# Optimization experiments

Measured on AMD Instinct MI355X. Metric: run time of the kernel, lower is better.

## Reference

```python
import jax, jax.numpy as jnp
import numpy as np
import math

B, L = 2, 512
D_MODEL = 64
N_HEAD = 8
N_GLOBAL = 64
N_ITER = 2
DISTS = 4
K_RANK = 4
REG_H = 1.0
REG_Z = 1.0
NEG = -1e9


def setup_inputs() -> dict:
    key = jax.random.key(0)
    k1, k2, k3, k4 = jax.random.split(key, 4)
    x = jax.random.normal(k1, (B, L, D_MODEL), dtype=jnp.float32)
    mask = jnp.ones((B, L), dtype=jnp.int32)
    # nn.init.normal_ defaults (std=1)
    distribution_params = jax.random.normal(k2, (2 * DISTS, K_RANK), dtype=jnp.float32)
    ternary = jax.random.normal(k3, (K_RANK, D_MODEL, D_MODEL, N_HEAD), dtype=jnp.float32)
    # global_: std = 1/sqrt(d_model), single-channel -> heads dim = 1
    global_param = jax.random.normal(k4, (N_GLOBAL, D_MODEL, 1), dtype=jnp.float32) * (1.0 / math.sqrt(D_MODEL))
    return {"x": x, "mask": mask, "distribution_params": distribution_params,
            "ternary": ternary, "global_param": global_param}


def _softmax(s):
    return jax.nn.softmax(s, axis=-1)


def _distmask(distribution_params, n, dtype):
    # distance(i,j) = clip(i - j, -dists, dists); row 0 of params is zeros (distance 0)
    dist = jnp.arange(n)[:, None] - jnp.arange(n)[None, :]
    dist = jnp.clip(dist, -DISTS, DISTS)
    params = jnp.concatenate([jnp.zeros((1, K_RANK), dtype), distribution_params], axis=0)  # [2*dists+1, k]
    # torch negative indexing wraps; emulate explicitly
    idx = jnp.where(dist < 0, dist + 2 * DISTS + 1, dist)
    return params[idx].transpose(2, 0, 1)  # [k, n, n]


def reference(x, mask, distribution_params, ternary, global_param):
    bsz, n, d = x.shape
    mask1d = mask != 0                                   # [B, L]
    mask2d = mask1d[:, :, None] & mask1d[:, None, :]     # [B, L, L]
    inv2d = ~mask2d[:, None, :, :]                       # [B, 1, L, L] broadcast over heads
    inv1d = ~mask1d[:, None, :, None]                    # [B, 1, L, 1]

    distmask = _distmask(distribution_params, n, x.dtype)  # [k, L, L]

    unary = x
    q_z = unary
    for _ in range(N_ITER):
        # --- normalize Z beliefs (softmax over d_model states) ---
        Q_z = _softmax(q_z / REG_Z)                      # [B, L, d]
        # precompute decomposed tensor messages: M1[z,k,j,a,c] = sum_b Qz[z,j,b] T[k,a,b,c]
        M1 = jnp.einsum('zjb,kabc->zkjac', Q_z, ternary)  # [B, k, L, d, h]
        # --- H update (each head of token i picks a parent j) ---
        # s_h[z,c,i,j] = sum_{a,k} Qz[z,i,a] M1[z,k,j,a,c] distmask[k,i,j]
        s_h = jnp.einsum('zia,zkjac,kij->zcij', Q_z, M1, distmask)  # [B, h, L, L]
        s_h = jnp.where(inv2d, NEG, s_h)
        Q_h = _softmax(s_h / REG_H)                      # softmax over parents j
        # --- global H update (single channel): token i picks one of n_global global nodes ---
        s_g = jnp.einsum('zia,gac->zcig', Q_z, global_param)        # [B, 1, L, G]
        s_g = jnp.where(inv1d, NEG, s_g)
        Q_g = _softmax(s_g / REG_H)
        # --- Z update: messages from ternary factors in both roles + global factor ---
        g1 = jnp.einsum('zcij,zkjac,kij->zia', Q_h, M1, distmask)   # token as Z_i
        M2 = jnp.einsum('zjb,kbac->zkjac', Q_z, ternary)            # swapped roles
        g2 = jnp.einsum('zcji,zkjac,kji->zia', Q_h, M2, distmask)   # token as Z_j
        gg = jnp.einsum('zcig,gac->zia', Q_g, global_param)         # global message
        q_z = unary + g1 + g2 + gg
        # damping=0, stepsize=1 -> plain full update
    # output_prob=False -> unnormalized scores
    return q_z
```

## Files before the change

### kernel.cpp

```cpp
#include <hip/hip_runtime.h>

#define BB 2
#define LL 512
#define DD 64
#define HH 8
#define GG 64
#define KK 4
#define NEGV -1e9f
#define NSLOT 36

typedef unsigned short ushort_t;
typedef __attribute__((ext_vector_type(8))) short bf16x8;
typedef __attribute__((ext_vector_type(4))) float f32x4;
#define MFMA(a, b, c) __builtin_amdgcn_mfma_f32_16x16x32_bf16(a, b, c, 0, 0, 0)

typedef const __attribute__((address_space(1))) unsigned int* gptr_t;
typedef __attribute__((address_space(3))) unsigned int* lptr_t;

__device__ __forceinline__ ushort_t f2b(float f) {
    unsigned int u = __float_as_uint(f);
    return (ushort_t)((u + 0x7FFFu + ((u >> 16) & 1u)) >> 16);
}
__device__ __forceinline__ float b2f(ushort_t s) {
    return __uint_as_float(((unsigned int)s) << 16);
}

__device__ __forceinline__ void gll16(const ushort_t* g, const ushort_t* l) {
    __builtin_amdgcn_global_load_lds(
        (gptr_t)(unsigned long long)g,
        (lptr_t)(unsigned int)(unsigned long long)l,
        16, 0, 0);
}

__device__ __forceinline__ void stage64a(ushort_t* dst, const ushort_t* src,
                                         int rowstride, int tid) {
    int lane = tid & 63, w = tid >> 6;
#pragma unroll
    for (int h = 0; h < 2; ++h) {
        int g = h * 256 + w * 64 + lane;
        int row = g >> 3, colg = g & 7;
        gll16(src + (size_t)row * rowstride + ((colg ^ (row & 7)) << 3),
              dst + (size_t)(h * 256 + w * 64) * 8);
    }
}
__device__ __forceinline__ bf16x8 frag(const ushort_t* s, int row, int col) {
    return *reinterpret_cast<const bf16x8*>(&s[(row << 6) + ((((col >> 3) ^ (row & 7))) << 3)]);
}
__device__ __forceinline__ bf16x8 maskfrag(bf16x8 v, int cnt, bool keep_prefix) {
    bf16x8 r;
#pragma unroll
    for (int u = 0; u < 8; ++u) {
        bool keep = keep_prefix ? (u < cnt) : (u >= cnt);
        r[u] = keep ? v[u] : (short)0;
    }
    return r;
}
__device__ __forceinline__ int iclamp(int v, int lo, int hi) {
    return v < lo ? lo : (v > hi ? hi : v);
}

__global__ __launch_bounds__(256) void k_prepT(const float* __restrict__ T,
                                               ushort_t* __restrict__ TB1,
                                               ushort_t* __restrict__ TB2) {
    int k = blockIdx.x >> 3, c = blockIdx.x & 7;
    int tid = threadIdx.x;
    for (int g = tid; g < 512; g += 256) {
        int a = g >> 3, b0 = (g & 7) * 8;
        ushort_t o1[8], o2[8];
#pragma unroll
        for (int u = 0; u < 8; ++u) {
            o1[u] = f2b(T[(((k * 64 + a) * 64) + b0 + u) * 8 + c]);
            o2[u] = f2b(T[(((k * 64 + b0 + u) * 64) + a) * 8 + c]);
        }
        size_t base = ((size_t)(k * 8 + c) * 64 + a) * 64 + b0;
        *reinterpret_cast<uint4*>(&TB1[base]) = *reinterpret_cast<uint4*>(o1);
        *reinterpret_cast<uint4*>(&TB2[base]) = *reinterpret_cast<uint4*>(o2);
    }
}

__global__ __launch_bounds__(256) void k_softmax_qz(const float* __restrict__ src,
                                                    float* __restrict__ Qz,
                                                    ushort_t* __restrict__ QzB) {
    int row = blockIdx.x * 4 + (threadIdx.x >> 6);
    int lane = threadIdx.x & 63;
    float v = src[row * DD + lane];
    float m = v;
#pragma unroll
    for (int o = 32; o > 0; o >>= 1) m = fmaxf(m, __shfl_xor(m, o, 64));
    float e = __expf(v - m);
    float s = e;
#pragma unroll
    for (int o = 32; o > 0; o >>= 1) s += __shfl_xor(s, o, 64);
    float r = e / s;
    Qz[row * DD + lane] = r;
    QzB[row * DD + lane] = f2b(r);
}

__global__ __launch_bounds__(256) void k_compute_M(const ushort_t* __restrict__ QzB,
        const ushort_t* __restrict__ TB1, const ushort_t* __restrict__ TB2,
        ushort_t* __restrict__ M1Nb, ushort_t* __restrict__ M2Nb) {
    int jt = blockIdx.x, c = blockIdx.y;
    int z = blockIdx.z >> 2, k = blockIdx.z & 3;
    __shared__ __align__(16) ushort_t sQ[4096], sB1[4096], sB2[4096];
    int tid = threadIdx.x;
    stage64a(sQ, QzB + (size_t)(z * LL + jt * 64) * DD, DD, tid);
    size_t tb = (size_t)(k * 8 + c) * 4096;
    stage64a(sB1, TB1 + tb, 64, tid);
    stage64a(sB2, TB2 + tb, 64, tid);
    __syncthreads();
    int w = tid >> 6, lm = tid & 15, lg = (tid & 63) >> 4;
    f32x4 a1[4], a2[4];
#pragma unroll
    for (int nf = 0; nf < 4; ++nf) { a1[nf] = {0.f,0.f,0.f,0.f}; a2[nf] = {0.f,0.f,0.f,0.f}; }
#pragma unroll
    for (int ks = 0; ks < 2; ++ks) {
        int kc = ks * 32 + lg * 8;
        bf16x8 af = frag(sQ, w * 16 + lm, kc);
#pragma unroll
        for (int nf = 0; nf < 4; ++nf) {
            a1[nf] = MFMA(af, frag(sB1, nf * 16 + lm, kc), a1[nf]);
            a2[nf] = MFMA(af, frag(sB2, nf * 16 + lm, kc), a2[nf]);
        }
    }
    size_t base = (((size_t)z * KK + k) * HH + c) * LL;
#pragma unroll
    for (int nf = 0; nf < 4; ++nf)
#pragma unroll
        for (int r = 0; r < 4; ++r) {
            int j = jt * 64 + w * 16 + lg * 4 + r;
            int a = nf * 16 + lm;
            M1Nb[(base + j) * DD + a] = f2b(a1[nf][r]);
            M2Nb[(base + j) * DD + a] = f2b(a2[nf][r]);
        }
}

__global__ __launch_bounds__(256, 4) void k_collaux(const float* __restrict__ Qz,
        const ushort_t* __restrict__ M1Nb, const ushort_t* __restrict__ M2Nb,
        const float* __restrict__ dp, const float* __restrict__ gp, const int* __restrict__ mask,
        ushort_t* __restrict__ MPNb, ushort_t* __restrict__ MMNb,
        ushort_t* __restrict__ MP2Nb, ushort_t* __restrict__ MM2Nb,
        ushort_t* __restrict__ MPT, ushort_t* __restrict__ MMT,
        ushort_t* __restrict__ MP2T, ushort_t* __restrict__ MM2T,
        float* __restrict__ BAND, float* __restrict__ QG) {
    __shared__ __align__(16) ushort_t sT[4 * 64 * 65];
    int tid = threadIdx.x;
    int b = blockIdx.x;
    if (b < 128) {
        int jt = b & 7, zc = b >> 3;
        int z = zc >> 3, c = zc & 7;
        ushort_t* sP1 = sT;
        ushort_t* sM1 = sT + 64 * 65;
        ushort_t* sP2 = sT + 2 * 64 * 65;
        ushort_t* sM2 = sT + 3 * 64 * 65;
        float w4[4], w5[4];
#pragma unroll
        for (int k = 0; k < 4; ++k) { w4[k] = dp[12 + k]; w5[k] = dp[16 + k]; }
        size_t b0 = (((size_t)z * KK * HH + c) * LL + jt * 64) * DD;
        const size_t kstr = (size_t)HH * LL * DD;
        for (int g = tid; g < 512; g += 256) {
            int j = g >> 3, a0 = (g & 7) * 8;
            size_t o = b0 + (size_t)j * DD + a0;
            float p1[8] = {}, q1[8] = {}, p2[8] = {}, q2[8] = {};
#pragma unroll
            for (int k = 0; k < 4; ++k) {
                uint4 v1 = *reinterpret_cast<const uint4*>(&M1Nb[o + k * kstr]);
                uint4 v2 = *reinterpret_cast<const uint4*>(&M2Nb[o + k * kstr]);
                const ushort_t* s1 = reinterpret_cast<const ushort_t*>(&v1);
                const ushort_t* s2 = reinterpret_cast<const ushort_t*>(&v2);
#pragma unroll
                for (int u = 0; u < 8; ++u) {
                    float f1 = b2f(s1[u]), f2v = b2f(s2[u]);
                    p1[u] += w4[k] * f1; q1[u] += w5[k] * f1;
                    p2[u] += w4[k] * f2v; q2[u] += w5[k] * f2v;
                }
            }
            ushort_t t1[8], t2[8], t3[8], t4[8];
#pragma unroll
            for (int u = 0; u < 8; ++u) {
                t1[u] = f2b(p1[u]); t2[u] = f2b(q1[u]); t3[u] = f2b(p2[u]); t4[u] = f2b(q2[u]);
                sP1[(a0 + u) * 65 + j] = t1[u]; sM1[(a0 + u) * 65 + j] = t2[u];
                sP2[(a0 + u) * 65 + j] = t3[u]; sM2[(a0 + u) * 65 + j] = t4[u];
            }
            size_t on = ((size_t)zc * LL + jt * 64 + j) * DD + a0;
            *reinterpret_cast<uint4*>(&MPNb[on])  = *reinterpret_cast<uint4*>(t1);
            *reinterpret_cast<uint4*>(&MMNb[on])  = *reinterpret_cast<uint4*>(t2);
            *reinterpret_cast<uint4*>(&MP2Nb[on]) = *reinterpret_cast<uint4*>(t3);
            *reinterpret_cast<uint4*>(&MM2Nb[on]) = *reinterpret_cast<uint4*>(t4);
        }
        __syncthreads();
        for (int g = tid; g < 512; g += 256) {
            int a = g >> 3, j0 = (g & 7) * 8;
            ushort_t o1[8], o2[8], o3[8], o4[8];
#pragma unroll
            for (int u = 0; u < 8; ++u) {
                o1[u] = sP1[a * 65 + j0 + u]; o2[u] = sM1[a * 65 + j0 + u];
                o3[u] = sP2[a * 65 + j0 + u]; o4[u] = sM2[a * 65 + j0 + u];
            }
            size_t ot = ((size_t)zc * DD + a) * LL + jt * 64 + j0;
            *reinterpret_cast<uint4*>(&MPT[ot])  = *reinterpret_cast<uint4*>(o1);
            *reinterpret_cast<uint4*>(&MMT[ot])  = *reinterpret_cast<uint4*>(o2);
            *reinterpret_cast<uint4*>(&MP2T[ot]) = *reinterpret_cast<uint4*>(o3);
            *reinterpret_cast<uint4*>(&MM2T[ot]) = *reinterpret_cast<uint4*>(o4);
        }
    } else if (b < 2176) {
        int w = (b - 128) * 4 + (tid >> 6);
        int lane = tid & 63;
        int j = w & 511, c = (w >> 9) & 7, z = w >> 12;
        float m[4];
#pragma unroll
        for (int k = 0; k < 4; ++k)
            m[k] = b2f(M1Nb[((((size_t)z * KK + k) * HH + c) * LL + j) * DD + lane]);
        float out = 0.f;
#pragma unroll
        for (int d = -3; d <= 3; ++d) {
            int i = j + d;
            if (i < 0 || i >= LL) continue;
            int idx = d < 0 ? d + 9 : d;
            float t = 0.f;
            if (idx != 0) {
#pragma unroll
                for (int k = 0; k < 4; ++k) t += dp[(idx - 1) * 4 + k] * m[k];
            }
            float s = Qz[(z * LL + i) * DD + lane] * t;
#pragma unroll
            for (int o = 32; o > 0; o >>= 1) s += __shfl_xor(s, o, 64);
            if (lane == d + 3) out = s;
        }
        if (lane < 7) BAND[(size_t)w * 8 + lane] = out;
    } else {
        float* gpS = reinterpret_cast<float*>(sT);
#pragma unroll
        for (int idx = tid; idx < 4096; idx += 256) gpS[(idx >> 6) * 68 + (idx & 63)] = gp[idx];
        __syncthreads();
        int row = (b - 2176) * 4 + (tid >> 6);
        int g = tid & 63;
        float qv = Qz[row * DD + g];
        float s = 0.f;
#pragma unroll 8
        for (int a = 0; a < 64; ++a) s += __shfl(qv, a, 64) * gpS[g * 68 + a];
        if (mask[row] == 0) s = NEGV;
        float m = s;
#pragma unroll
        for (int o = 32; o > 0; o >>= 1) m = fmaxf(m, __shfl_xor(m, o, 64));
        float e = __expf(s - m);
        float sum = e;
#pragma unroll
        for (int o = 32; o > 0; o >>= 1) sum += __shfl_xor(sum, o, 64);
        QG[row * GG + g] = e / sum;
    }
}

__global__ __launch_bounds__(256, 2) void k_shsm32(const ushort_t* __restrict__ QzB,
        const ushort_t* __restrict__ MPNb, const ushort_t* __restrict__ MMNb,
        const float* __restrict__ BAND, const int* __restrict__ mask,
        ushort_t* __restrict__ SHB, ushort_t* __restrict__ SHBT) {
    int ih = blockIdx.x, zc = blockIdx.y;
    int it = ih >> 1, rh = ih & 1;
    int z = zc >> 3;
    int R0 = it * 64 + rh * 32;
    __shared__ __align__(16) ushort_t sA[2048];
    __shared__ __align__(16) ushort_t sB0[4096], sB1[4096], sBd[4096];
    __shared__ __align__(16) ushort_t tl[2][32 * 72];
    __shared__ float redA[2][32], redB[2][32];
    int tid = threadIdx.x;
    int w = tid >> 6, lm = tid & 15, lg = (tid & 63) >> 4;
    int rw = w & 1, cw = w >> 1;
    {
        int row = tid >> 3, colg = tid & 7;
        gll16(&QzB[(size_t)(z * LL + R0 + row) * DD + ((colg ^ (row & 7)) << 3)],
              sA + (size_t)(w * 64) * 8);
    }
    f32x4 acc[4][4];
#pragma unroll
    for (int jl = 0; jl < 4; ++jl)
#pragma unroll
        for (int nf = 0; nf < 4; ++nf) acc[jl][nf] = {0.f, 0.f, 0.f, 0.f};
    int dstep = it & 3;
#pragma unroll
    for (int s = 0; s < 4; ++s) {
        __syncthreads();
        int jt0 = s, jt1 = 4 + s;
        const ushort_t* src0 = (it >= jt0) ? MPNb : MMNb;
        const ushort_t* src1 = (it >= jt1) ? MPNb : MMNb;
        stage64a(sB0, src0 + ((size_t)zc * LL + jt0 * 64) * DD, DD, tid);
        stage64a(sB1, src1 + ((size_t)zc * LL + jt1 * 64) * DD, DD, tid);
        if (s == dstep)
            stage64a(sBd, MMNb + ((size_t)zc * LL + it * 64) * DD, DD, tid);
        __syncthreads();
        int jtg = cw ? jt1 : jt0;
        const ushort_t* sBx = cw ? sB1 : sB0;
#pragma unroll
        for (int ks = 0; ks < 2; ++ks) {
            int kc = ks * 32 + lg * 8;
            bf16x8 af = frag(sA, rw * 16 + lm, kc);
#pragma unroll
            for (int nf = 0; nf < 4; ++nf)
                acc[s][nf] = MFMA(af, frag(sBx, nf * 16 + lm, kc), acc[s][nf]);
        }
        if (jtg == it) {
            f32x4 accM[4];
#pragma unroll
            for (int nf = 0; nf < 4; ++nf) accM[nf] = {0.f, 0.f, 0.f, 0.f};
#pragma unroll
            for (int ks = 0; ks < 2; ++ks) {
                int kc = ks * 32 + lg * 8;
                bf16x8 af = frag(sA, rw * 16 + lm, kc);
#pragma unroll
                for (int nf = 0; nf < 4; ++nf)
                    accM[nf] = MFMA(af, frag(sBd, nf * 16 + lm, kc), accM[nf]);
            }
#pragma unroll
            for (int nf = 0; nf < 4; ++nf)
#pragma unroll
                for (int r = 0; r < 4; ++r) {
                    int i = R0 + rw * 16 + lg * 4 + r;
                    int j = it * 64 + nf * 16 + lm;
                    if (i <= j) acc[s][nf][r] = accM[nf][r];
                }
        }
    }
    int mi[4];
#pragma unroll
    for (int r = 0; r < 4; ++r) mi[r] = mask[z * LL + R0 + rw * 16 + lg * 4 + r];
#pragma unroll
    for (int jl = 0; jl < 4; ++jl) {
        int jtg = cw * 4 + jl;
#pragma unroll
        for (int nf = 0; nf < 4; ++nf) {
            int j = jtg * 64 + nf * 16 + lm;
            int mjv = mask[z * LL + j];
#pragma unroll
            for (int r = 0; r < 4; ++r) {
                int i = R0 + rw * 16 + lg * 4 + r;
                int d = i - j;
                float v = acc[jl][nf][r];
                if (d >= -3 && d <= 3) v = BAND[((size_t)zc * LL + j) * 8 + (d + 3)];
                if (!(mi[r] && mjv)) v = NEGV;
                acc[jl][nf][r] = v;
            }
        }
    }
    float gm[4], gs[4], inv[4];
#pragma unroll
    for (int r = 0; r < 4; ++r) {
        float m = -1e30f;
#pragma unroll
        for (int jl = 0; jl < 4; ++jl)
#pragma unroll
            for (int nf = 0; nf < 4; ++nf) m = fmaxf(m, acc[jl][nf][r]);
#pragma unroll
        for (int o = 1; o < 16; o <<= 1) m = fmaxf(m, __shfl_xor(m, o, 64));
        gm[r] = m;
    }
    if (lm == 0) {
#pragma unroll
        for (int r = 0; r < 4; ++r) redA[cw][rw * 16 + lg * 4 + r] = gm[r];
    }
    __syncthreads();
#pragma unroll
    for (int r = 0; r < 4; ++r)
        gm[r] = fmaxf(gm[r], redA[cw ^ 1][rw * 16 + lg * 4 + r]);
#pragma unroll
    for (int r = 0; r < 4; ++r) {
        float s = 0.f;
#pragma unroll
        for (int jl = 0; jl < 4; ++jl)
#pragma unroll
            for (int nf = 0; nf < 4; ++nf) {
                float e = __expf(acc[jl][nf][r] - gm[r]);
                acc[jl][nf][r] = e;
                s += e;
            }
#pragma unroll
        for (int o = 1; o < 16; o <<= 1) s += __shfl_xor(s, o, 64);
        gs[r] = s;
    }
    if (lm == 0) {
#pragma unroll
        for (int r = 0; r < 4; ++r) redB[cw][rw * 16 + lg * 4 + r] = gs[r];
    }
    __syncthreads();
#pragma unroll
    for (int r = 0; r < 4; ++r)
        inv[r] = 1.f / (gs[r] + redB[cw ^ 1][rw * 16 + lg * 4 + r]);
#pragma unroll
    for (int jl = 0; jl < 4; ++jl) {
        __syncthreads();
#pragma unroll
        for (int nf = 0; nf < 4; ++nf)
#pragma unroll
            for (int r = 0; r < 4; ++r)
                tl[cw][(rw * 16 + lg * 4 + r) * 72 + nf * 16 + lm] =
                    f2b(acc[jl][nf][r] * inv[r]);
        __syncthreads();
#pragma unroll
        for (int g = tid; g < 512; g += 256) {
            int cwg = g >> 8, rem = g & 255;
            int jtg = cwg * 4 + jl;
            int i_loc = rem >> 3, gj = rem & 7;
            ushort_t tmp[8];
#pragma unroll
            for (int u = 0; u < 8; ++u) tmp[u] = tl[cwg][i_loc * 72 + gj * 8 + u];
            *reinterpret_cast<uint4*>(
                &SHB[((size_t)zc * LL + R0 + i_loc) * LL + jtg * 64 + gj * 8]) =
                *reinterpret_cast<uint4*>(tmp);
        }
#pragma unroll
        for (int g = tid; g < 512; g += 256) {
            int cwg = g >> 8, rem = g & 255;
            int jtg = cwg * 4 + jl;
            int j_loc = rem >> 2, gi = rem & 3;
            ushort_t tmp2[8];
#pragma unroll
            for (int u = 0; u < 8; ++u) tmp2[u] = tl[cwg][(gi * 8 + u) * 72 + j_loc];
            *reinterpret_cast<uint4*>(
                &SHBT[((size_t)zc * LL + jtg * 64 + j_loc) * LL + R0 + gi * 8]) =
                *reinterpret_cast<uint4*>(tmp2);
        }
    }
}

__global__ __launch_bounds__(256, 4) void k_g12corr(const ushort_t* __restrict__ SHB,
        const ushort_t* __restrict__ SHBT,
        const ushort_t* __restrict__ MPT, const ushort_t* __restrict__ MMT,
        const ushort_t* __restrict__ MP2T, const ushort_t* __restrict__ MM2T,
        const ushort_t* __restrict__ M1Nb, const ushort_t* __restrict__ M2Nb,
        const ushort_t* __restrict__ MPNb, const ushort_t* __restrict__ MMNb,
        const ushort_t* __restrict__ MP2Nb, const ushort_t* __restrict__ MM2Nb,
        const float* __restrict__ dp, float* __restrict__ PG) {
    __shared__ __align__(16) ushort_t sSH[4096], sM[4096];
    int tid = threadIdx.x;
    int b = blockIdx.x;
    if (b < 512) {
        int it = b & 7, jc = (b >> 3) & 1, zcw = b >> 4;
        int which = zcw >> 4;
        int z = (zcw >> 3) & 1, c = zcw & 7;
        const ushort_t* Amat = which ? SHBT : SHB;
        const ushort_t* TP = which ? MP2T : MPT;
        const ushort_t* TM = which ? MM2T : MMT;
        int w = tid >> 6, lm = tid & 15, lg = (tid & 63) >> 4;
        f32x4 acc[4];
#pragma unroll
        for (int nf = 0; nf < 4; ++nf) acc[nf] = {0.f,0.f,0.f,0.f};
        size_t shbase = ((size_t)(z * HH + c) * LL + it * 64) * LL;
        size_t mbase  = ((size_t)(z * HH + c) * DD) * LL;
        for (int js = 0; js < 4; ++js) {
            int j0 = jc * 256 + js * 64;
            bool dg = (j0 == it * 64);
            bool useP = which == 0 ? (j0 < it * 64) : (j0 > it * 64);
            __syncthreads();
            stage64a(sSH, Amat + shbase + j0, LL, tid);
            stage64a(sM, (dg ? TP : (useP ? TP : TM)) + mbase + j0, LL, tid);
            __syncthreads();
            for (int pass = 0; pass < (dg ? 2 : 1); ++pass) {
                if (pass == 1) {
                    __syncthreads();
                    stage64a(sM, TM + mbase + j0, LL, tid);
                    __syncthreads();
                }
#pragma unroll
                for (int ks = 0; ks < 2; ++ks) {
                    int kc = ks * 32 + lg * 8;
                    int jb = j0 + kc;
                    bf16x8 af = frag(sSH, w * 16 + lm, kc);
                    if (dg) {
                        int i = it * 64 + w * 16 + lm;
                        int cnt = (which == 0) ? iclamp(i - jb, 0, 8) : iclamp(i + 1 - jb, 0, 8);
                        af = maskfrag(af, cnt, (pass == 0) == (which == 0));
                    }
#pragma unroll
                    for (int nf = 0; nf < 4; ++nf)
                        acc[nf] = MFMA(af, frag(sM, nf * 16 + lm, kc), acc[nf]);
                }
            }
        }
        int slot = which * 16 + c * 2 + jc;
#pragma unroll
        for (int nf = 0; nf < 4; ++nf)
#pragma unroll
            for (int r = 0; r < 4; ++r) {
                int i = it * 64 + w * 16 + lg * 4 + r;
                int a = nf * 16 + lm;
                PG[((size_t)(slot * BB + z) * LL + i) * DD + a] = acc[nf][r];
            }
    } else {
        int bid = b - 512;
        int which = bid >> 9; bid &= 511;
        int w = bid * 4 + (tid >> 6);
        int lane = tid & 63;
        int ch = w & 1, i = (w >> 1) & 511, z = w >> 10;
        const ushort_t* Mx = which ? M2Nb : M1Nb;
        const ushort_t* MPb = which ? MP2Nb : MPNb;
        const ushort_t* MMb = which ? MM2Nb : MMNb;
        float acc = 0.f;
        for (int cc = 0; cc < 4; ++cc) {
            int c = ch * 4 + cc;
#pragma unroll
            for (int d = -3; d <= 3; ++d) {
                int j = which ? i + d : i - d;
                if (j < 0 || j >= LL) continue;
                float qh = which ? b2f(SHB[(((size_t)z * HH + c) * LL + j) * LL + i])
                                 : b2f(SHB[(((size_t)z * HH + c) * LL + i) * LL + j]);
                int idx = d < 0 ? d + 9 : d;
                float e = 0.f;
                if (idx != 0) {
#pragma unroll
                    for (int k = 0; k < 4; ++k)
                        e += dp[(idx - 1) * 4 + k] *
                             b2f(Mx[((((size_t)z * KK + k) * HH + c) * LL + j) * DD + lane]);
                }
                const ushort_t* mb = (d > 0) ? MPb : MMb;
                float mn = b2f(mb[(((size_t)z * HH + c) * LL + j) * DD + lane]);
                acc += qh * (e - mn);
            }
        }
        int slot = 32 + which * 2 + ch;
        PG[(((size_t)slot * BB + z) * LL + i) * DD + lane] = acc;
    }
}

__global__ __launch_bounds__(256) void k_update_sm(const float* __restrict__ x,
                         const float* __restrict__ PG, const float* __restrict__ QG,
                         const float* __restrict__ gp,
                         float* __restrict__ Qz, ushort_t* __restrict__ QzB) {
    __shared__ __align__(16) float gpS[64][68];
    int tid = threadIdx.x;
#pragma unroll
    for (int idx = tid; idx < 4096; idx += 256) gpS[idx >> 6][idx & 63] = gp[idx];
    __syncthreads();
    int row = blockIdx.x * 4 + (tid >> 6);
    int a = tid & 63;
    float acc = x[row * DD + a];
    float qgv = QG[row * GG + a];
#pragma unroll 8
    for (int g = 0; g < 64; ++g) acc += __shfl(qgv, g, 64) * gpS[g][a];
#pragma unroll 6
    for (int s = 0; s < NSLOT; ++s) acc += PG[((size_t)s * BB * LL + row) * DD + a];
    float m = acc;
#pragma unroll
    for (int o = 32; o > 0; o >>= 1) m = fmaxf(m, __shfl_xor(m, o, 64));
    float e = __expf(acc - m);
    float s2 = e;
#pragma unroll
    for (int o = 32; o > 0; o >>= 1) s2 += __shfl_xor(s2, o, 64);
    float r = e / s2;
    Qz[row * DD + a] = r;
    QzB[row * DD + a] = f2b(r);
}

__global__ __launch_bounds__(256) void k_update_fin(const float* __restrict__ x,
                         const float* __restrict__ PG, const float* __restrict__ QG,
                         const float* __restrict__ gp, float* __restrict__ outq) {
    __shared__ __align__(16) float gpS[64][68];
    int tid = threadIdx.x;
#pragma unroll
    for (int idx = tid; idx < 4096; idx += 256) gpS[idx >> 6][idx & 63] = gp[idx];
    __syncthreads();
    int row = blockIdx.x * 4 + (tid >> 6);
    int a = tid & 63;
    float acc = x[row * DD + a];
    float qgv = QG[row * GG + a];
#pragma unroll 8
    for (int g = 0; g < 64; ++g) acc += __shfl(qgv, g, 64) * gpS[g][a];
#pragma unroll 6
    for (int s = 0; s < NSLOT; ++s) acc += PG[((size_t)s * BB * LL + row) * DD + a];
    outq[row * DD + a] = acc;
}

extern "C" void kernel_launch(void* const* d_in, const int* in_sizes, int n_in,
                              void* d_out, int out_size, void* d_ws, size_t ws_size,
                              hipStream_t stream) {
    const float* x    = (const float*)d_in[0];
    const int*   mask = (const int*)d_in[1];
    const float* dp   = (const float*)d_in[2];
    const float* T    = (const float*)d_in[3];
    const float* gp   = (const float*)d_in[4];
    float* out = (float*)d_out;

    float* p = (float*)d_ws;
    float* Qz = p;                        p += 65536;
    ushort_t* QzB = (ushort_t*)p;         p += 32768;
    ushort_t* TB1 = (ushort_t*)p;         p += 65536;
    ushort_t* TB2 = (ushort_t*)p;         p += 65536;
    ushort_t* M1Nb = (ushort_t*)p;        p += 1048576;
    ushort_t* M2Nb = (ushort_t*)p;        p += 1048576;
    ushort_t* MPNb  = (ushort_t*)p;       p += 262144;
    ushort_t* MMNb  = (ushort_t*)p;       p += 262144;
    ushort_t* MP2Nb = (ushort_t*)p;       p += 262144;
    ushort_t* MM2Nb = (ushort_t*)p;       p += 262144;
    ushort_t* MPT   = (ushort_t*)p;       p += 262144;
    ushort_t* MMT   = (ushort_t*)p;       p += 262144;
    ushort_t* MP2T  = (ushort_t*)p;       p += 262144;
    ushort_t* MM2T  = (ushort_t*)p;       p += 262144;
    float* BAND = p;                      p += 65536;
    ushort_t* SHB  = (ushort_t*)p;        p += 2097152;
    ushort_t* SHBT = (ushort_t*)p;        p += 2097152;
    float* QG   = p;                      p += 65536;
    float* PG   = p;                      p += (size_t)NSLOT * 65536;

    hipLaunchKernelGGL(k_prepT, dim3(32), dim3(256), 0, stream, T, TB1, TB2);
    hipLaunchKernelGGL(k_softmax_qz, dim3(256), dim3(256), 0, stream, x, Qz, QzB);

    for (int iter = 0; iter < 2; ++iter) {
        hipLaunchKernelGGL(k_compute_M, dim3(8, 8, 8), dim3(256), 0, stream, QzB, TB1, TB2, M1Nb, M2Nb);
        hipLaunchKernelGGL(k_collaux, dim3(2432), dim3(256), 0, stream, Qz, M1Nb, M2Nb, dp, gp, mask,
                           MPNb, MMNb, MP2Nb, MM2Nb, MPT, MMT, MP2T, MM2T, BAND, QG);
        hipLaunchKernelGGL(k_shsm32, dim3(16, 16), dim3(256), 0, stream, QzB, MPNb, MMNb, BAND, mask,
                           SHB, SHBT);
        hipLaunchKernelGGL(k_g12corr, dim3(1536), dim3(256), 0, stream, SHB, SHBT,
                           MPT, MMT, MP2T, MM2T, M1Nb, M2Nb,
                           MPNb, MMNb, MP2Nb, MM2Nb, dp, PG);
        if (iter == 0)
            hipLaunchKernelGGL(k_update_sm, dim3(256), dim3(256), 0, stream, x, PG, QG, gp, Qz, QzB);
        else
            hipLaunchKernelGGL(k_update_fin, dim3(256), dim3(256), 0, stream, x, PG, QG, gp, out);
    }
}
```

Measured before the change: 134.4 us.

## Fuse M computation with k-collapse and double-buffer LDS staging in downstream kernels

Merges the M1/M2 MFMA kernel with the k-weighted collapse into one kernel. Each block loops over the four ranks, accumulates the distance-weighted sums in registers, and writes both the normal and transposed collapsed tensors, so M1/M2 no longer have to be reread from global memory. The band/global-score work moves into a separate smaller kernel. It also adds double-buffered LDS prefetching in k_shsm32 and k_g12corr, which drops one barrier per step, and flattens the diagonal two-pass case into a linear subtile schedule. The cost is fewer blocks in the fused kernel (128) and more LDS per block.

```diff
diff --git a/kernel.cpp b/kernel.cpp
--- a/kernel.cpp
+++ b/kernel.cpp
@@ -96,114 +96,120 @@
     QzB[row * DD + lane] = f2b(r);
 }
 
-__global__ __launch_bounds__(256) void k_compute_M(const ushort_t* __restrict__ QzB,
+__global__ __launch_bounds__(256, 2) void k_Mcoll(const ushort_t* __restrict__ QzB,
         const ushort_t* __restrict__ TB1, const ushort_t* __restrict__ TB2,
-        ushort_t* __restrict__ M1Nb, ushort_t* __restrict__ M2Nb) {
-    int jt = blockIdx.x, c = blockIdx.y;
-    int z = blockIdx.z >> 2, k = blockIdx.z & 3;
-    __shared__ __align__(16) ushort_t sQ[4096], sB1[4096], sB2[4096];
-    int tid = threadIdx.x;
-    stage64a(sQ, QzB + (size_t)(z * LL + jt * 64) * DD, DD, tid);
-    size_t tb = (size_t)(k * 8 + c) * 4096;
-    stage64a(sB1, TB1 + tb, 64, tid);
-    stage64a(sB2, TB2 + tb, 64, tid);
-    __syncthreads();
-    int w = tid >> 6, lm = tid & 15, lg = (tid & 63) >> 4;
-    f32x4 a1[4], a2[4];
-#pragma unroll
-    for (int nf = 0; nf < 4; ++nf) { a1[nf] = {0.f,0.f,0.f,0.f}; a2[nf] = {0.f,0.f,0.f,0.f}; }
-#pragma unroll
-    for (int ks = 0; ks < 2; ++ks) {
-        int kc = ks * 32 + lg * 8;
-        bf16x8 af = frag(sQ, w * 16 + lm, kc);
-#pragma unroll
-        for (int nf = 0; nf < 4; ++nf) {
-            a1[nf] = MFMA(af, frag(sB1, nf * 16 + lm, kc), a1[nf]);
-            a2[nf] = MFMA(af, frag(sB2, nf * 16 + lm, kc), a2[nf]);
-        }
-    }
-    size_t base = (((size_t)z * KK + k) * HH + c) * LL;
-#pragma unroll
-    for (int nf = 0; nf < 4; ++nf)
-#pragma unroll
-        for (int r = 0; r < 4; ++r) {
-            int j = jt * 64 + w * 16 + lg * 4 + r;
-            int a = nf * 16 + lm;
-            M1Nb[(base + j) * DD + a] = f2b(a1[nf][r]);
-            M2Nb[(base + j) * DD + a] = f2b(a2[nf][r]);
-        }
-}
-
-__global__ __launch_bounds__(256, 4) void k_collaux(const float* __restrict__ Qz,
-        const ushort_t* __restrict__ M1Nb, const ushort_t* __restrict__ M2Nb,
-        const float* __restrict__ dp, const float* __restrict__ gp, const int* __restrict__ mask,
+        const float* __restrict__ dp,
+        ushort_t* __restrict__ M1Nb, ushort_t* __restrict__ M2Nb,
         ushort_t* __restrict__ MPNb, ushort_t* __restrict__ MMNb,
         ushort_t* __restrict__ MP2Nb, ushort_t* __restrict__ MM2Nb,
         ushort_t* __restrict__ MPT, ushort_t* __restrict__ MMT,
-        ushort_t* __restrict__ MP2T, ushort_t* __restrict__ MM2T,
+        ushort_t* __restrict__ MP2T, ushort_t* __restrict__ MM2T) {
+    int jt = blockIdx.x, zc = blockIdx.y;
+    int z = zc >> 3, c = zc & 7;
+    __shared__ __align__(16) ushort_t smem[20480];
+    ushort_t* sQ = smem;
+    int tid = threadIdx.x;
+    stage64a(sQ, QzB + (size_t)(z * LL + jt * 64) * DD, DD, tid);
+    stage64a(smem + 4096,  TB1 + (size_t)(0 * 8 + c) * 4096, 64, tid);
+    stage64a(smem + 12288, TB2 + (size_t)(0 * 8 + c) * 4096, 64, tid);
+    int w = tid >> 6, lm = tid & 15, lg = (tid & 63) >> 4;
+    float w4[4], w5[4];
+#pragma unroll
+    for (int k = 0; k < 4; ++k) { w4[k] = dp[12 + k]; w5[k] = dp[16 + k]; }
+    f32x4 cp1[4], cm1[4], cp2[4], cm2[4];
+#pragma unroll
+    for (int nf = 0; nf < 4; ++nf) {
+        cp1[nf] = {0.f,0.f,0.f,0.f}; cm1[nf] = {0.f,0.f,0.f,0.f};
+        cp2[nf] = {0.f,0.f,0.f,0.f}; cm2[nf] = {0.f,0.f,0.f,0.f};
+    }
+#pragma unroll
+    for (int k = 0; k < 4; ++k) {
+        __syncthreads();
+        if (k < 3) {
+            ushort_t* nb1 = smem + (((k + 1) & 1) ? 8192 : 4096);
+            ushort_t* nb2 = smem + (((k + 1) & 1) ? 16384 : 12288);
+            stage64a(nb1, TB1 + (size_t)((k + 1) * 8 + c) * 4096, 64, tid);
+            stage64a(nb2, TB2 + (size_t)((k + 1) * 8 + c) * 4096, 64, tid);
+        }
+        const ushort_t* b1 = smem + ((k & 1) ? 8192 : 4096);
+        const ushort_t* b2 = smem + ((k & 1) ? 16384 : 12288);
+        f32x4 a1[4], a2[4];
+#pragma unroll
+        for (int nf = 0; nf < 4; ++nf) { a1[nf] = {0.f,0.f,0.f,0.f}; a2[nf] = {0.f,0.f,0.f,0.f}; }
+#pragma unroll
+        for (int ks = 0; ks < 2; ++ks) {
+            int kc = ks * 32 + lg * 8;
+            bf16x8 af = frag(sQ, w * 16 + lm, kc);
+#pragma unroll
+            for (int nf = 0; nf < 4; ++nf) {
+                a1[nf] = MFMA(af, frag(b1, nf * 16 + lm, kc), a1[nf]);
+                a2[nf] = MFMA(af, frag(b2, nf * 16 + lm, kc), a2[nf]);
+            }
+        }
+        size_t base = (((size_t)z * KK + k) * HH + c) * LL;
+#pragma unroll
+        for (int nf = 0; nf < 4; ++nf)
+#pragma unroll
+            for (int r = 0; r < 4; ++r) {
+                int j = jt * 64 + w * 16 + lg * 4 + r;
+                int a = nf * 16 + lm;
+                float v1 = a1[nf][r], v2 = a2[nf][r];
+                M1Nb[(base + j) * DD + a] = f2b(v1);
+                M2Nb[(base + j) * DD + a] = f2b(v2);
+                cp1[nf][r] += w4[k] * v1; cm1[nf][r] += w5[k] * v1;
+                cp2[nf][r] += w4[k] * v2; cm2[nf][r] += w5[k] * v2;
+            }
+    }
+#pragma unroll
+    for (int nf = 0; nf < 4; ++nf)
+#pragma unroll
+        for (int r = 0; r < 4; ++r) {
+            int jl = w * 16 + lg * 4 + r;
+            int a = nf * 16 + lm;
+            size_t on = ((size_t)zc * LL + jt * 64 + jl) * DD + a;
+            MPNb[on]  = f2b(cp1[nf][r]); MMNb[on]  = f2b(cm1[nf][r]);
+            MP2Nb[on] = f2b(cp2[nf][r]); MM2Nb[on] = f2b(cm2[nf][r]);
+        }
+    __syncthreads();
+    ushort_t* tr0 = smem;
+    ushort_t* tr1 = smem + 4224;
+    ushort_t* tr2 = smem + 8448;
+    ushort_t* tr3 = smem + 12672;
+#pragma unroll
+    for (int nf = 0; nf < 4; ++nf)
+#pragma unroll
+        for (int r = 0; r < 4; ++r) {
+            int jl = w * 16 + lg * 4 + r;
+            int a = nf * 16 + lm;
+            tr0[a * 66 + jl] = f2b(cp1[nf][r]); tr1[a * 66 + jl] = f2b(cm1[nf][r]);
+            tr2[a * 66 + jl] = f2b(cp2[nf][r]); tr3[a * 66 + jl] = f2b(cm2[nf][r]);
+        }
+    __syncthreads();
+    for (int g = tid; g < 512; g += 256) {
+        int a = g >> 3, j0 = (g & 7) * 8;
+        ushort_t o1[8], o2[8], o3[8], o4[8];
+#pragma unroll
+        for (int u = 0; u < 8; ++u) {
+            o1[u] = tr0[a * 66 + j0 + u]; o2[u] = tr1[a * 66 + j0 + u];
+            o3[u] = tr2[a * 66 + j0 + u]; o4[u] = tr3[a * 66 + j0 + u];
+        }
+        size_t ot = ((size_t)zc * DD + a) * LL + jt * 64 + j0;
+        *reinterpret_cast<uint4*>(&MPT[ot])  = *reinterpret_cast<uint4*>(o1);
+        *reinterpret_cast<uint4*>(&MMT[ot])  = *reinterpret_cast<uint4*>(o2);
+        *reinterpret_cast<uint4*>(&MP2T[ot]) = *reinterpret_cast<uint4*>(o3);
+        *reinterpret_cast<uint4*>(&MM2T[ot]) = *reinterpret_cast<uint4*>(o4);
+    }
+}
+
+__global__ __launch_bounds__(256, 4) void k_bandqg(const float* __restrict__ Qz,
+        const ushort_t* __restrict__ M1Nb,
+        const float* __restrict__ dp, const float* __restrict__ gp, const int* __restrict__ mask,
         float* __restrict__ BAND, float* __restrict__ QG) {
-    __shared__ __align__(16) ushort_t sT[4 * 64 * 65];
+    __shared__ __align__(16) float gpS[64 * 68];
     int tid = threadIdx.x;
     int b = blockIdx.x;
-    if (b < 128) {
-        int jt = b & 7, zc = b >> 3;
-        int z = zc >> 3, c = zc & 7;
-        ushort_t* sP1 = sT;
-        ushort_t* sM1 = sT + 64 * 65;
-        ushort_t* sP2 = sT + 2 * 64 * 65;
-        ushort_t* sM2 = sT + 3 * 64 * 65;
-        float w4[4], w5[4];
-#pragma unroll
-        for (int k = 0; k < 4; ++k) { w4[k] = dp[12 + k]; w5[k] = dp[16 + k]; }
-        size_t b0 = (((size_t)z * KK * HH + c) * LL + jt * 64) * DD;
-        const size_t kstr = (size_t)HH * LL * DD;
-        for (int g = tid; g < 512; g += 256) {
-            int j = g >> 3, a0 = (g & 7) * 8;
-            size_t o = b0 + (size_t)j * DD + a0;
-            float p1[8] = {}, q1[8] = {}, p2[8] = {}, q2[8] = {};
-#pragma unroll
-            for (int k = 0; k < 4; ++k) {
-                uint4 v1 = *reinterpret_cast<const uint4*>(&M1Nb[o + k * kstr]);
-                uint4 v2 = *reinterpret_cast<const uint4*>(&M2Nb[o + k * kstr]);
-                const ushort_t* s1 = reinterpret_cast<const ushort_t*>(&v1);
-                const ushort_t* s2 = reinterpret_cast<const ushort_t*>(&v2);
-#pragma unroll
-                for (int u = 0; u < 8; ++u) {
-                    float f1 = b2f(s1[u]), f2v = b2f(s2[u]);
-                    p1[u] += w4[k] * f1; q1[u] += w5[k] * f1;
-                    p2[u] += w4[k] * f2v; q2[u] += w5[k] * f2v;
-                }
-            }
-            ushort_t t1[8], t2[8], t3[8], t4[8];
-#pragma unroll
-            for (int u = 0; u < 8; ++u) {
-                t1[u] = f2b(p1[u]); t2[u] = f2b(q1[u]); t3[u] = f2b(p2[u]); t4[u] = f2b(q2[u]);
-                sP1[(a0 + u) * 65 + j] = t1[u]; sM1[(a0 + u) * 65 + j] = t2[u];
-                sP2[(a0 + u) * 65 + j] = t3[u]; sM2[(a0 + u) * 65 + j] = t4[u];
-            }
-            size_t on = ((size_t)zc * LL + jt * 64 + j) * DD + a0;
-            *reinterpret_cast<uint4*>(&MPNb[on])  = *reinterpret_cast<uint4*>(t1);
-            *reinterpret_cast<uint4*>(&MMNb[on])  = *reinterpret_cast<uint4*>(t2);
-            *reinterpret_cast<uint4*>(&MP2Nb[on]) = *reinterpret_cast<uint4*>(t3);
-            *reinterpret_cast<uint4*>(&MM2Nb[on]) = *reinterpret_cast<uint4*>(t4);
-        }
-        __syncthreads();
-        for (int g = tid; g < 512; g += 256) {
-            int a = g >> 3, j0 = (g & 7) * 8;
-            ushort_t o1[8], o2[8], o3[8], o4[8];
-#pragma unroll
-            for (int u = 0; u < 8; ++u) {
-                o1[u] = sP1[a * 65 + j0 + u]; o2[u] = sM1[a * 65 + j0 + u];
-                o3[u] = sP2[a * 65 + j0 + u]; o4[u] = sM2[a * 65 + j0 + u];
-            }
-            size_t ot = ((size_t)zc * DD + a) * LL + jt * 64 + j0;
-            *reinterpret_cast<uint4*>(&MPT[ot])  = *reinterpret_cast<uint4*>(o1);
-            *reinterpret_cast<uint4*>(&MMT[ot])  = *reinterpret_cast<uint4*>(o2);
-            *reinterpret_cast<uint4*>(&MP2T[ot]) = *reinterpret_cast<uint4*>(o3);
-            *reinterpret_cast<uint4*>(&MM2T[ot]) = *reinterpret_cast<uint4*>(o4);
-        }
-    } else if (b < 2176) {
-        int w = (b - 128) * 4 + (tid >> 6);
+    if (b < 2048) {
+        int w = b * 4 + (tid >> 6);
         int lane = tid & 63;
         int j = w & 511, c = (w >> 9) & 7, z = w >> 12;
         float m[4];
@@ -228,11 +234,10 @@
         }
         if (lane < 7) BAND[(size_t)w * 8 + lane] = out;
     } else {
-        float* gpS = reinterpret_cast<float*>(sT);
 #pragma unroll
         for (int idx = tid; idx < 4096; idx += 256) gpS[(idx >> 6) * 68 + (idx & 63)] = gp[idx];
         __syncthreads();
-        int row = (b - 2176) * 4 + (tid >> 6);
+        int row = (b - 2048) * 4 + (tid >> 6);
         int g = tid & 63;
         float qv = Qz[row * DD + g];
         float s = 0.f;
@@ -259,7 +264,8 @@
     int z = zc >> 3;
     int R0 = it * 64 + rh * 32;
     __shared__ __align__(16) ushort_t sA[2048];
-    __shared__ __align__(16) ushort_t sB0[4096], sB1[4096], sBd[4096];
+    __shared__ __align__(16) ushort_t sBd[4096];
+    __shared__ __align__(16) ushort_t sB[2][8192];
     __shared__ __align__(16) ushort_t tl[2][32 * 72];
     __shared__ float redA[2][32], redB[2][32];
     int tid = threadIdx.x;
@@ -270,25 +276,27 @@
         gll16(&QzB[(size_t)(z * LL + R0 + row) * DD + ((colg ^ (row & 7)) << 3)],
               sA + (size_t)(w * 64) * 8);
     }
+    stage64a(sBd, MMNb + ((size_t)zc * LL + it * 64) * DD, DD, tid);
+    stage64a(sB[0], ((it >= 0) ? MPNb : MMNb) + ((size_t)zc * LL + 0 * 64) * DD, DD, tid);
+    stage64a(sB[0] + 4096, ((it >= 4) ? MPNb : MMNb) + ((size_t)zc * LL + 4 * 64) * DD, DD, tid);
     f32x4 acc[4][4];
 #pragma unroll
     for (int jl = 0; jl < 4; ++jl)
 #pragma unroll
         for (int nf = 0; nf < 4; ++nf) acc[jl][nf] = {0.f, 0.f, 0.f, 0.f};
-    int dstep = it & 3;
 #pragma unroll
     for (int s = 0; s < 4; ++s) {
         __syncthreads();
+        if (s < 3) {
+            int jt0n = s + 1, jt1n = 5 + s;
+            stage64a(sB[(s + 1) & 1],
+                     ((it >= jt0n) ? MPNb : MMNb) + ((size_t)zc * LL + jt0n * 64) * DD, DD, tid);
+            stage64a(sB[(s + 1) & 1] + 4096,
+                     ((it >= jt1n) ? MPNb : MMNb) + ((size_t)zc * LL + jt1n * 64) * DD, DD, tid);
+        }
         int jt0 = s, jt1 = 4 + s;
-        const ushort_t* src0 = (it >= jt0) ? MPNb : MMNb;
-        const ushort_t* src1 = (it >= jt1) ? MPNb : MMNb;
-        stage64a(sB0, src0 + ((size_t)zc * LL + jt0 * 64) * DD, DD, tid);
-        stage64a(sB1, src1 + ((size_t)zc * LL + jt1 * 64) * DD, DD, tid);
-        if (s == dstep)
-            stage64a(sBd, MMNb + ((size_t)zc * LL + it * 64) * DD, DD, tid);
-        __syncthreads();
         int jtg = cw ? jt1 : jt0;
-        const ushort_t* sBx = cw ? sB1 : sB0;
+        const ushort_t* sBx = sB[s & 1] + (cw ? 4096 : 0);
 #pragma unroll
         for (int ks = 0; ks < 2; ++ks) {
             int kc = ks * 32 + lg * 8;
@@ -428,7 +436,7 @@
         const ushort_t* __restrict__ MPNb, const ushort_t* __restrict__ MMNb,
         const ushort_t* __restrict__ MP2Nb, const ushort_t* __restrict__ MM2Nb,
         const float* __restrict__ dp, float* __restrict__ PG) {
-    __shared__ __align__(16) ushort_t sSH[4096], sM[4096];
+    __shared__ __align__(16) ushort_t sSH[2][4096], sM[2][4096];
     int tid = threadIdx.x;
     int b = blockIdx.x;
     if (b < 512) {
@@ -439,39 +447,60 @@
         const ushort_t* TP = which ? MP2T : MPT;
         const ushort_t* TM = which ? MM2T : MMT;
         int w = tid >> 6, lm = tid & 15, lg = (tid & 63) >> 4;
-        f32x4 acc[4];
-#pragma unroll
-        for (int nf = 0; nf < 4; ++nf) acc[nf] = {0.f,0.f,0.f,0.f};
         size_t shbase = ((size_t)(z * HH + c) * LL + it * 64) * LL;
         size_t mbase  = ((size_t)(z * HH + c) * DD) * LL;
-        for (int js = 0; js < 4; ++js) {
+        int dgjs = ((it >> 2) == jc) ? (it & 3) : 99;
+        int ns = (dgjs < 4) ? 5 : 4;
+        auto getsub = [&](int t, const ushort_t*& shp, const ushort_t*& mp,
+                          int& j0v, int& passv) {
+            int js, pass;
+            if (dgjs > 3)            { js = t;        pass = -1; }
+            else if (t < dgjs)       { js = t;        pass = -1; }
+            else if (t == dgjs)      { js = t;        pass = 0;  }
+            else if (t == dgjs + 1)  { js = dgjs;     pass = 1;  }
+            else                     { js = t - 1;    pass = -1; }
             int j0 = jc * 256 + js * 64;
-            bool dg = (j0 == it * 64);
-            bool useP = which == 0 ? (j0 < it * 64) : (j0 > it * 64);
+            bool useP = (pass == -1)
+                        ? (which == 0 ? (j0 < it * 64) : (j0 > it * 64))
+                        : (pass == 0);
+            shp = Amat + shbase + j0;
+            mp  = (useP ? TP : TM) + mbase + j0;
+            j0v = j0; passv = pass;
+        };
+        f32x4 acc[4];
+#pragma unroll
+        for (int nf = 0; nf < 4; ++nf) acc[nf] = {0.f,0.f,0.f,0.f};
+        {
+            const ushort_t *shp, *mp; int j0v, pv;
+            getsub(0, shp, mp, j0v, pv);
+            stage64a(sSH[0], shp, LL, tid);
+            stage64a(sM[0], mp, LL, tid);
+        }
+        for (int t = 0; t < ns; ++t) {
             __syncthreads();
-            stage64a(sSH, Amat + shbase + j0, LL, tid);
-            stage64a(sM, (dg ? TP : (useP ? TP : TM)) + mbase + j0, LL, tid);
-            __syncthreads();
-            for (int pass = 0; pass < (dg ? 2 : 1); ++pass) {
-                if (pass == 1) {
-                    __syncthreads();
-                    stage64a(sM, TM + mbase + j0, LL, tid);
-                    __syncthreads();
+            if (t + 1 < ns) {
+                const ushort_t *shp, *mp; int j0v, pv;
+                getsub(t + 1, shp, mp, j0v, pv);
+                stage64a(sSH[(t + 1) & 1], shp, LL, tid);
+                stage64a(sM[(t + 1) & 1], mp, LL, tid);
+            }
+            const ushort_t *shp_, *mp_; int j0v, pv;
+            getsub(t, shp_, mp_, j0v, pv);
+            const ushort_t* sshx = sSH[t & 1];
+            const ushort_t* smx = sM[t & 1];
+#pragma unroll
+            for (int ks = 0; ks < 2; ++ks) {
+                int kc = ks * 32 + lg * 8;
+                int jb = j0v + kc;
+                bf16x8 af = frag(sshx, w * 16 + lm, kc);
+                if (pv >= 0) {
+                    int i = it * 64 + w * 16 + lm;
+                    int cnt = (which == 0) ? iclamp(i - jb, 0, 8) : iclamp(i + 1 - jb, 0, 8);
+                    af = maskfrag(af, cnt, (pv == 0) == (which == 0));
                 }
 #pragma unroll
-                for (int ks = 0; ks < 2; ++ks) {
-                    int kc = ks * 32 + lg * 8;
-                    int jb = j0 + kc;
-                    bf16x8 af = frag(sSH, w * 16 + lm, kc);
-                    if (dg) {
-                        int i = it * 64 + w * 16 + lm;
-                        int cnt = (which == 0) ? iclamp(i - jb, 0, 8) : iclamp(i + 1 - jb, 0, 8);
-                        af = maskfrag(af, cnt, (pass == 0) == (which == 0));
-                    }
-#pragma unroll
-                    for (int nf = 0; nf < 4; ++nf)
-                        acc[nf] = MFMA(af, frag(sM, nf * 16 + lm, kc), acc[nf]);
-                }
+                for (int nf = 0; nf < 4; ++nf)
+                    acc[nf] = MFMA(af, frag(smx, nf * 16 + lm, kc), acc[nf]);
             }
         }
         int slot = which * 16 + c * 2 + jc;
@@ -602,9 +631,10 @@
     hipLaunchKernelGGL(k_softmax_qz, dim3(256), dim3(256), 0, stream, x, Qz, QzB);
 
     for (int iter = 0; iter < 2; ++iter) {
-        hipLaunchKernelGGL(k_compute_M, dim3(8, 8, 8), dim3(256), 0, stream, QzB, TB1, TB2, M1Nb, M2Nb);
-        hipLaunchKernelGGL(k_collaux, dim3(2432), dim3(256), 0, stream, Qz, M1Nb, M2Nb, dp, gp, mask,
-                           MPNb, MMNb, MP2Nb, MM2Nb, MPT, MMT, MP2T, MM2T, BAND, QG);
+        hipLaunchKernelGGL(k_Mcoll, dim3(8, 16), dim3(256), 0, stream, QzB, TB1, TB2, dp,
+                           M1Nb, M2Nb, MPNb, MMNb, MP2Nb, MM2Nb, MPT, MMT, MP2T, MM2T);
+        hipLaunchKernelGGL(k_bandqg, dim3(2304), dim3(256), 0, stream, Qz, M1Nb, dp, gp, mask,
+                           BAND, QG);
         hipLaunchKernelGGL(k_shsm32, dim3(16, 16), dim3(256), 0, stream, QzB, MPNb, MMNb, BAND, mask,
                            SHB, SHBT);
         hipLaunchKernelGGL(k_g12corr, dim3(1536), dim3(256), 0, stream, SHB, SHBT,
```

After: 135.6 us. About the same (+1.0%).
